# Kernel optimization log

Measured on AMD Instinct MI355X. Metric: run time of the kernel, lower is better.

The kernel has to match this reference:

```python
import jax, jax.numpy as jnp
import numpy as np

B, N, C, NH = 4, 2304, 256, 8
HD = C // NH            # head dim = 32
HS = WS = 48            # H = W = sqrt(N)
RADIUS = 3.0
MLP_HID = 4 * C
SCALE = HD ** (-0.5)
NEG = -1e9              # stands in for -inf (identical softmax up to fp eps)
EPS = 1e-6


def spatial_mask():
    # get_spatial_mask: cdist of (y, x) grid coords, -inf where dist > radius
    yy, xx = jnp.meshgrid(jnp.arange(HS), jnp.arange(WS), indexing='ij')
    coords = jnp.stack([yy, xx], -1).reshape(-1, 2).astype(jnp.float32)  # [N, 2]
    d2 = jnp.sum((coords[:, None, :] - coords[None, :, :]) ** 2, -1)     # [N, N]
    return jnp.where(d2 > RADIUS * RADIUS, NEG, 0.0)


def layernorm(x, g, b):
    mu = jnp.mean(x, -1, keepdims=True)
    var = jnp.mean((x - mu) ** 2, -1, keepdims=True)
    return (x - mu) * jax.lax.rsqrt(var + EPS) * g + b


def setup_inputs() -> dict:
    key = jax.random.key(0)
    ks = jax.random.split(key, 16)
    s = 0.02
    return {
        'x':    jax.random.normal(ks[0], (B, N, C), jnp.float32),
        'x_kv': jax.random.normal(ks[1], (B, N, C), jnp.float32),
        'Wq': jax.random.normal(ks[2], (C, C), jnp.float32) * s,
        'bq': jnp.zeros((C,), jnp.float32),
        'Wk': jax.random.normal(ks[3], (C, C), jnp.float32) * s,
        'bk': jnp.zeros((C,), jnp.float32),
        'Wv': jax.random.normal(ks[4], (C, C), jnp.float32) * s,
        'bv': jnp.zeros((C,), jnp.float32),
        'Wp': jax.random.normal(ks[5], (C, C), jnp.float32) * s,
        'bp': jnp.zeros((C,), jnp.float32),
        'g1': jnp.ones((C,), jnp.float32),
        'b1': jnp.zeros((C,), jnp.float32),
        'g2': jnp.ones((C,), jnp.float32),
        'b2': jnp.zeros((C,), jnp.float32),
        'W1': jax.random.normal(ks[6], (C, MLP_HID), jnp.float32) * s,
        'bm1': jnp.zeros((MLP_HID,), jnp.float32),
        'W2': jax.random.normal(ks[7], (MLP_HID, C), jnp.float32) * s,
        'bm2': jnp.zeros((C,), jnp.float32),
    }


def reference(x, x_kv, Wq, bq, Wk, bk, Wv, bv, Wp, bp,
              g1, b1, g2, b2, W1, bm1, W2, bm2):
    mask = spatial_mask()                                  # [N, N]
    h = layernorm(x, g1, b1)
    hkv = layernorm(x_kv, g1, b1)
    q = (h @ Wq + bq).reshape(B, N, NH, HD)
    k = (hkv @ Wk + bk).reshape(B, N, NH, HD)
    v = (hkv @ Wv + bv).reshape(B, N, NH, HD)
    scores = jnp.einsum('bqhd,bkhd->bhqk', q, k) * SCALE + mask
    attn = jax.nn.softmax(scores, axis=-1)
    out = jnp.einsum('bhqk,bkhd->bqhd', attn, v).reshape(B, N, C)
    x = x + out @ Wp + bp
    m = layernorm(x, g2, b2)
    x = x + jax.nn.gelu(m @ W1 + bm1, approximate=False) @ W2 + bm2
    return x
```

## Files before the change

kernel.cpp:

```cpp
#include <hip/hip_runtime.h>
#include <hip/hip_fp16.h>
#include <math.h>

#define BB 4
#define NN 2304
#define CC 256
#define HS 48
#define HID 1024
#define BNROWS (BB * NN)
#define ATTN_SCALE 0.17677669529663687f

typedef _Float16 f16;
typedef __attribute__((ext_vector_type(2))) _Float16 h2;
typedef __attribute__((ext_vector_type(8))) _Float16 h8;
typedef __attribute__((ext_vector_type(4))) float f4;

#define GLLS16(g, l)                                                        \
    __builtin_amdgcn_global_load_lds(                                       \
        (const __attribute__((address_space(1))) unsigned int*)(g),         \
        (__attribute__((address_space(3))) unsigned int*)(l), 16, 0, 0)
#define WAIT_VM0()   asm volatile("s_waitcnt vmcnt(0)" ::: "memory")
#define WAIT_VM6()   asm volatile("s_waitcnt vmcnt(6)" ::: "memory")
#define WAIT_LGKM0() asm volatile("s_waitcnt lgkmcnt(0)" ::: "memory")

static __device__ __forceinline__ float wave_sum64(float v) {
    v += __shfl_xor(v, 32, 64);
    v += __shfl_xor(v, 16, 64);
    v += __shfl_xor(v, 8, 64);
    v += __shfl_xor(v, 4, 64);
    v += __shfl_xor(v, 2, 64);
    v += __shfl_xor(v, 1, 64);
    return v;
}

static __device__ __forceinline__ int xcd_swizzle_lin() {
    const int gx = (int)gridDim.x;
    const int lin = (int)blockIdx.y * gx + (int)blockIdx.x;
    const int nwg = gx * (int)gridDim.y;
    return (nwg & 7) ? lin : ((lin & 7) * (nwg >> 3) + (lin >> 3));
}

__global__ __launch_bounds__(256) void prep_ln1_kernel(
    const float* __restrict__ x, const float* __restrict__ xkv,
    const float* __restrict__ Wq, const float* __restrict__ Wk,
    const float* __restrict__ Wv, const float* __restrict__ Wp,
    const float* __restrict__ W1, const float* __restrict__ W2,
    const float* __restrict__ bq, const float* __restrict__ bk,
    const float* __restrict__ bv,
    const float* __restrict__ g, const float* __restrict__ be,
    f16* __restrict__ WqkvT, f16* __restrict__ WpT,
    f16* __restrict__ W1T, f16* __restrict__ W2T, float* __restrict__ bqkv,
    f16* __restrict__ hq, f16* __restrict__ hkv)
{
    __shared__ float tt[32][33];
    int bx = blockIdx.x;
    const int tid = threadIdx.x;
    if (bx < 768) {
        const float* src; f16* dst; int K, N;
        if (bx < 64)        { src = Wq; dst = WqkvT;           K = 256;  N = 256; }
        else if (bx < 128)  { src = Wk; dst = WqkvT + 65536;   K = 256;  N = 256;  bx -= 64; }
        else if (bx < 192)  { src = Wv; dst = WqkvT + 131072;  K = 256;  N = 256;  bx -= 128; }
        else if (bx < 256)  { src = Wp; dst = WpT;             K = 256;  N = 256;  bx -= 192; }
        else if (bx < 512)  { src = W1; dst = W1T;             K = 256;  N = 1024; bx -= 256; }
        else                { src = W2; dst = W2T;             K = 1024; N = 256;  bx -= 512; }
        const int tN = N >> 5;
        const int kt = bx / tN, nt = bx - kt * tN;
        const int rr = tid >> 5, cc = tid & 31;
#pragma unroll
        for (int j = 0; j < 4; ++j)
            tt[rr + 8 * j][cc] = src[(size_t)(kt * 32 + rr + 8 * j) * N + nt * 32 + cc];
        __syncthreads();
#pragma unroll
        for (int j = 0; j < 4; ++j)
            dst[(size_t)(nt * 32 + rr + 8 * j) * K + kt * 32 + cc] = (f16)tt[cc][rr + 8 * j];
        return;
    }
    if (bx == 768) {
        if (tid < 256) {
            bqkv[tid]       = bq[tid];
            bqkv[tid + 256] = bk[tid];
            bqkv[tid + 512] = bv[tid];
        }
        return;
    }
    const int r = (bx - 769) * 4 + (tid >> 6);
    const int lane = tid & 63;
    const float* src; f16* dst;
    if (r < BNROWS) { src = x + (size_t)r * CC;              dst = hq + (size_t)r * CC; }
    else { src = xkv + (size_t)(r - BNROWS) * CC; dst = hkv + (size_t)(r - BNROWS) * CC; }
    const float4 v = ((const float4*)src)[lane];
    const float mu = wave_sum64(v.x + v.y + v.z + v.w) * (1.0f / CC);
    const float d0 = v.x - mu, d1 = v.y - mu, d2 = v.z - mu, d3 = v.w - mu;
    const float var = wave_sum64(d0 * d0 + d1 * d1 + d2 * d2 + d3 * d3) * (1.0f / CC);
    const float rs = rsqrtf(var + 1e-6f);
    const float4 g4 = ((const float4*)g)[lane];
    const float4 b4 = ((const float4*)be)[lane];
    h2 o01 = (h2){(f16)(d0 * rs * g4.x + b4.x), (f16)(d1 * rs * g4.y + b4.y)};
    h2 o23 = (h2){(f16)(d2 * rs * g4.z + b4.z), (f16)(d3 * rs * g4.w + b4.w)};
    ((h2*)dst)[lane * 2] = o01;
    ((h2*)dst)[lane * 2 + 1] = o23;
}

template <bool GELU, int RESID, bool OUTF32, bool QKV>
__global__ __launch_bounds__(256, 4) void gemm_wave(
    const f16* __restrict__ Aq, const f16* __restrict__ Akv,
    const f16* __restrict__ Bt, const float* __restrict__ bias,
    const void* __restrict__ resid, void* __restrict__ out1,
    void* __restrict__ outkv, int N, int K)
{
    __shared__ f16 lds[4 * 6144];
    const int tid = threadIdx.x;
    const int wid = tid >> 6, lane = tid & 63;
    const int ln15 = lane & 15, quad = lane >> 4;
    const int jr = lane >> 2, js = lane & 3;
    f16* slot = lds + wid * 6144;
    const int sl = xcd_swizzle_lin();
    const int gx = (int)gridDim.x;
    const int bx = sl % gx, by = sl / gx;
    const int n0 = bx * 64;
    const int m0 = (by * 4 + wid) * 32;
    const f16* Ap = QKV ? (n0 < 256 ? Aq : Akv) : Aq;

    size_t ga[2], gb[4];
#pragma unroll
    for (int i = 0; i < 2; ++i) {
        const int r = i * 16 + jr;
        const int q = (js - (r >> 1)) & 3;
        ga[i] = (size_t)(m0 + r) * K + q * 8;
    }
#pragma unroll
    for (int i = 0; i < 4; ++i) {
        const int r = i * 16 + jr;
        const int q = (js - (r >> 1)) & 3;
        gb[i] = (size_t)(n0 + r) * K + q * 8;
    }
    int aoff[2], boff[4];
#pragma unroll
    for (int mt = 0; mt < 2; ++mt) {
        const int r = mt * 16 + ln15;
        aoff[mt] = (r * 4 + ((quad + (r >> 1)) & 3)) * 16;
    }
#pragma unroll
    for (int nt = 0; nt < 4; ++nt) {
        const int r = nt * 16 + ln15;
        boff[nt] = (r * 4 + ((quad + (r >> 1)) & 3)) * 16;
    }

    f4 acc[2][4];
#pragma unroll
    for (int i = 0; i < 2; ++i)
#pragma unroll
        for (int j = 0; j < 4; ++j) acc[i][j] = (f4){0.f, 0.f, 0.f, 0.f};

    {
        f16* Al = slot;
        f16* Bl = slot + 1024;
#pragma unroll
        for (int i = 0; i < 2; ++i) GLLS16(Ap + ga[i], Al + i * 512);
#pragma unroll
        for (int i = 0; i < 4; ++i) GLLS16(Bt + gb[i], Bl + i * 512);
    }

    int cur = 0;
    for (int k0 = 0; k0 < K; k0 += 32) {
        const bool more = (k0 + 32 < K);
        f16* Ac = slot + cur * 3072;
        f16* Bc = Ac + 1024;
        if (more) {
            f16* An = slot + (cur ^ 1) * 3072;
            f16* Bn = An + 1024;
            WAIT_LGKM0();
#pragma unroll
            for (int i = 0; i < 2; ++i) GLLS16(Ap + ga[i] + k0 + 32, An + i * 512);
#pragma unroll
            for (int i = 0; i < 4; ++i) GLLS16(Bt + gb[i] + k0 + 32, Bn + i * 512);
            WAIT_VM6();
        } else {
            WAIT_VM0();
        }
        h8 aF[2], bF[4];
#pragma unroll
        for (int nt = 0; nt < 4; ++nt)
            bF[nt] = *(const h8*)((const char*)Bc + boff[nt]);
#pragma unroll
        for (int mt = 0; mt < 2; ++mt)
            aF[mt] = *(const h8*)((const char*)Ac + aoff[mt]);
#pragma unroll
        for (int mt = 0; mt < 2; ++mt)
#pragma unroll
            for (int nt = 0; nt < 4; ++nt)
                acc[mt][nt] = __builtin_amdgcn_mfma_f32_16x16x32_f16(
                    aF[mt], bF[nt], acc[mt][nt], 0, 0, 0);
        cur ^= 1;
    }

    f16* qdst = nullptr; int qstr = 0, qn0 = 0;
    if (QKV) {
        if (n0 < 256) { qdst = (f16*)out1;  qstr = 256; qn0 = n0; }
        else          { qdst = (f16*)outkv; qstr = 512; qn0 = n0 - 256; }
    }
#pragma unroll
    for (int nt = 0; nt < 4; ++nt) {
        const int gn = n0 + nt * 16 + ln15;
        const float bs = bias[gn];
#pragma unroll
        for (int mt = 0; mt < 2; ++mt) {
#pragma unroll
            for (int r = 0; r < 4; ++r) {
                const int gm = m0 + mt * 16 + quad * 4 + r;
                float v = acc[mt][nt][r] + bs;
                if (GELU) v = 0.5f * v * (1.0f + erff(v * 0.70710678118654752f));
                if (RESID == 1) v += ((const float*)resid)[(size_t)gm * N + gn];
                if (RESID == 2) v += (float)((const f16*)resid)[(size_t)gm * N + gn];
                if (QKV) {
                    qdst[(size_t)gm * qstr + qn0 + nt * 16 + ln15] = (f16)v;
                } else if (OUTF32) {
                    ((float*)out1)[(size_t)gm * N + gn] = v;
                } else {
                    ((f16*)out1)[(size_t)gm * N + gn] = (f16)v;
                }
            }
        }
    }
}

__global__ __launch_bounds__(256, 3) void gemm_op_ln2(
    const f16* __restrict__ Aa, const f16* __restrict__ Bt,
    const float* __restrict__ bias, const float* __restrict__ xres,
    const float* __restrict__ g, const float* __restrict__ be,
    f16* __restrict__ x1, f16* __restrict__ m2)
{
    __shared__ f16 lds[4 * 6144];
    __shared__ float sred[32][4][2];
    const int tid = threadIdx.x;
    const int wid = tid >> 6, lane = tid & 63;
    const int ln15 = lane & 15, quad = lane >> 4;
    const int jr = lane >> 2, js = lane & 3;
    f16* slot = lds + wid * 6144;
    const int m0 = blockIdx.x * 32;
    const int n0 = wid * 64;
    const int K = 256;

    size_t ga[2], gb[4];
#pragma unroll
    for (int i = 0; i < 2; ++i) {
        const int r = i * 16 + jr;
        const int q = (js - (r >> 1)) & 3;
        ga[i] = (size_t)(m0 + r) * K + q * 8;
    }
#pragma unroll
    for (int i = 0; i < 4; ++i) {
        const int r = i * 16 + jr;
        const int q = (js - (r >> 1)) & 3;
        gb[i] = (size_t)(n0 + r) * K + q * 8;
    }
    int aoff[2], boff[4];
#pragma unroll
    for (int mt = 0; mt < 2; ++mt) {
        const int r = mt * 16 + ln15;
        aoff[mt] = (r * 4 + ((quad + (r >> 1)) & 3)) * 16;
    }
#pragma unroll
    for (int nt = 0; nt < 4; ++nt) {
        const int r = nt * 16 + ln15;
        boff[nt] = (r * 4 + ((quad + (r >> 1)) & 3)) * 16;
    }

    f4 acc[2][4];
#pragma unroll
    for (int i = 0; i < 2; ++i)
#pragma unroll
        for (int j = 0; j < 4; ++j) acc[i][j] = (f4){0.f, 0.f, 0.f, 0.f};

    {
        f16* Al = slot;
        f16* Bl = slot + 1024;
#pragma unroll
        for (int i = 0; i < 2; ++i) GLLS16(Aa + ga[i], Al + i * 512);
#pragma unroll
        for (int i = 0; i < 4; ++i) GLLS16(Bt + gb[i], Bl + i * 512);
    }
    int cur = 0;
    for (int k0 = 0; k0 < K; k0 += 32) {
        const bool more = (k0 + 32 < K);
        f16* Ac = slot + cur * 3072;
        f16* Bc = Ac + 1024;
        if (more) {
            f16* An = slot + (cur ^ 1) * 3072;
            f16* Bn = An + 1024;
            WAIT_LGKM0();
#pragma unroll
            for (int i = 0; i < 2; ++i) GLLS16(Aa + ga[i] + k0 + 32, An + i * 512);
#pragma unroll
            for (int i = 0; i < 4; ++i) GLLS16(Bt + gb[i] + k0 + 32, Bn + i * 512);
            WAIT_VM6();
        } else {
            WAIT_VM0();
        }
        h8 aF[2], bF[4];
#pragma unroll
        for (int nt = 0; nt < 4; ++nt)
            bF[nt] = *(const h8*)((const char*)Bc + boff[nt]);
#pragma unroll
        for (int mt = 0; mt < 2; ++mt)
            aF[mt] = *(const h8*)((const char*)Ac + aoff[mt]);
#pragma unroll
        for (int mt = 0; mt < 2; ++mt)
#pragma unroll
            for (int nt = 0; nt < 4; ++nt)
                acc[mt][nt] = __builtin_amdgcn_mfma_f32_16x16x32_f16(
                    aF[mt], bF[nt], acc[mt][nt], 0, 0, 0);
        cur ^= 1;
    }

    float bsv[4], g2v[4], b2v[4];
#pragma unroll
    for (int nt = 0; nt < 4; ++nt) {
        const int gn = n0 + nt * 16 + ln15;
        bsv[nt] = bias[gn];
        g2v[nt] = g[gn];
        b2v[nt] = be[gn];
    }
    float s1[2][4], s2[2][4];
#pragma unroll
    for (int mt = 0; mt < 2; ++mt)
#pragma unroll
        for (int r = 0; r < 4; ++r) { s1[mt][r] = 0.f; s2[mt][r] = 0.f; }
#pragma unroll
    for (int mt = 0; mt < 2; ++mt) {
#pragma unroll
        for (int r = 0; r < 4; ++r) {
            const int gm = m0 + mt * 16 + quad * 4 + r;
#pragma unroll
            for (int nt = 0; nt < 4; ++nt) {
                const int gn = n0 + nt * 16 + ln15;
                float v = acc[mt][nt][r] + bsv[nt]
                        + xres[(size_t)gm * CC + gn];
                acc[mt][nt][r] = v;
                x1[(size_t)gm * CC + gn] = (f16)v;
                s1[mt][r] += v;
                s2[mt][r] += v * v;
            }
        }
    }
#pragma unroll
    for (int off = 1; off < 16; off <<= 1) {
#pragma unroll
        for (int mt = 0; mt < 2; ++mt)
#pragma unroll
            for (int r = 0; r < 4; ++r) {
                s1[mt][r] += __shfl_xor(s1[mt][r], off, 64);
                s2[mt][r] += __shfl_xor(s2[mt][r], off, 64);
            }
    }
    if (ln15 == 0) {
#pragma unroll
        for (int mt = 0; mt < 2; ++mt)
#pragma unroll
            for (int r = 0; r < 4; ++r) {
                const int rr = mt * 16 + quad * 4 + r;
                sred[rr][wid][0] = s1[mt][r];
                sred[rr][wid][1] = s2[mt][r];
            }
    }
    __syncthreads();
#pragma unroll
    for (int mt = 0; mt < 2; ++mt) {
#pragma unroll
        for (int r = 0; r < 4; ++r) {
            const int rr = mt * 16 + quad * 4 + r;
            const int gm = m0 + rr;
            float a = 0.f, b = 0.f;
#pragma unroll
            for (int w = 0; w < 4; ++w) {
                a += sred[rr][w][0];
                b += sred[rr][w][1];
            }
            const float mu = a * (1.0f / CC);
            const float var = fmaxf(b * (1.0f / CC) - mu * mu, 0.0f);
            const float rs = rsqrtf(var + 1e-6f);
#pragma unroll
            for (int nt = 0; nt < 4; ++nt) {
                const int gn = n0 + nt * 16 + ln15;
                const float v = acc[mt][nt][r];
                m2[(size_t)gm * CC + gn] =
                    (f16)((v - mu) * rs * g2v[nt] + b2v[nt]);
            }
        }
    }
}

__device__ __constant__ int ATT_DY[29] = {
    -3, -2, -2, -2, -2, -2, -1, -1, -1, -1, -1, 0, 0, 0, 0,
    0, 0, 0, 1, 1, 1, 1, 1, 2, 2, 2, 2, 2, 3};
__device__ __constant__ int ATT_DX[29] = {
    0, -2, -1, 0, 1, 2, -2, -1, 0, 1, 2, -3, -2, -1, 0,
    1, 2, 3, -2, -1, 0, 1, 2, -2, -1, 0, 1, 2, 0};

__global__ __launch_bounds__(128) void attn_tile_kernel(
    const f16* __restrict__ qf, const f16* __restrict__ kvf,
    f16* __restrict__ ao)
{
    __shared__ f16 ks[196][66];
    __shared__ f16 vs[196][66];
    const int tile = blockIdx.x, hp = blockIdx.y, b = blockIdx.z;
    const int ty0 = (tile / 6) * 8, tx0 = (tile - (tile / 6) * 6) * 8;
    const int tid = threadIdx.x;

    const int q = tid & 63, hh = tid >> 6;
    const int qy = q >> 3, qx = q & 7;
    const size_t qrow = (size_t)b * NN + (ty0 + qy) * HS + tx0 + qx;
    const f16* qp = qf + qrow * CC + hp * 64 + hh * 32;
    uint4 qa[4];
#pragma unroll
    for (int i = 0; i < 4; ++i) qa[i] = ((const uint4*)qp)[i];

#pragma unroll
    for (int bt = 0; bt < 5; ++bt) {
        uint4 v[5];
        int rr[5], sg[5];
#pragma unroll
        for (int j = 0; j < 5; ++j) {
            const int it = bt * 5 + j;
            const int idx = tid + it * 128;
            const int r = idx >> 4, seg = idx & 15;
            rr[j] = r; sg[j] = seg;
            const int ry = r / 14;
            const int gy = ty0 - 3 + ry, gx = tx0 - 3 + (r - ry * 14);
            uint4 val = {0u, 0u, 0u, 0u};
            const bool act = (it < 24) || (tid < 64);
            if (act && (unsigned)gy < HS && (unsigned)gx < HS) {
                const size_t rowb = ((size_t)b * NN + gy * HS + gx) * 512;
                const int ch = (seg < 8) ? (hp * 64 + seg * 8)
                                         : (256 + hp * 64 + (seg - 8) * 8);
                val = *(const uint4*)&kvf[rowb + ch];
            }
            v[j] = val;
        }
#pragma unroll
        for (int j = 0; j < 5; ++j) {
            const int it = bt * 5 + j;
            if (it == 24 && tid >= 64) continue;
            f16* dstp = (sg[j] < 8) ? &ks[rr[j]][(sg[j] & 7) * 8]
                                    : &vs[rr[j]][(sg[j] & 7) * 8];
            ((unsigned int*)dstp)[0] = v[j].x;
            ((unsigned int*)dstp)[1] = v[j].y;
            ((unsigned int*)dstp)[2] = v[j].z;
            ((unsigned int*)dstp)[3] = v[j].w;
        }
    }
    __syncthreads();

    const h2* q2 = (const h2*)qa;

    float s[29];
#pragma unroll
    for (int n = 0; n < 29; ++n) {
        const int dy = ATT_DY[n], dx = ATT_DX[n];
        const int r = (qy + 3 + dy) * 14 + qx + 3 + dx;
        const bool valid = (unsigned)(ty0 + qy + dy) < HS &&
                           (unsigned)(tx0 + qx + dx) < HS;
        float a = 0.0f;
        const h2* kp = (const h2*)&ks[r][hh * 32];
#pragma unroll
        for (int i = 0; i < 16; ++i)
            a = __builtin_amdgcn_fdot2(q2[i], kp[i], a, false);
        s[n] = valid ? a * ATTN_SCALE : -1e30f;
    }
    float m = s[0];
#pragma unroll
    for (int n = 1; n < 29; ++n) m = fmaxf(m, s[n]);
    float l = 0.0f;
#pragma unroll
    for (int n = 0; n < 29; ++n) { s[n] = __expf(s[n] - m); l += s[n]; }
    h2 a2[16];
#pragma unroll
    for (int i = 0; i < 16; ++i) a2[i] = (h2){(f16)0.f, (f16)0.f};
#pragma unroll
    for (int n = 0; n < 29; ++n) {
        const int dy = ATT_DY[n], dx = ATT_DX[n];
        const int r = (qy + 3 + dy) * 14 + qx + 3 + dx;
        const f16 pn = (f16)s[n];
        const h2 ph = (h2){pn, pn};
        const h2* vp = (const h2*)&vs[r][hh * 32];
#pragma unroll
        for (int i = 0; i < 16; ++i) a2[i] += ph * vp[i];
    }
    const float inv = 1.0f / l;
    uint4 ov[4];
    f16* oh = (f16*)ov;
#pragma unroll
    for (int i = 0; i < 16; ++i) {
        oh[2 * i]     = (f16)((float)a2[i][0] * inv);
        oh[2 * i + 1] = (f16)((float)a2[i][1] * inv);
    }
    uint4* dst = (uint4*)(ao + qrow * CC + hp * 64 + hh * 32);
#pragma unroll
    for (int i = 0; i < 4; ++i) dst[i] = ov[i];
}

extern "C" void kernel_launch(void* const* d_in, const int* in_sizes, int n_in,
                              void* d_out, int out_size, void* d_ws, size_t ws_size,
                              hipStream_t stream) {
    const float* x    = (const float*)d_in[0];
    const float* x_kv = (const float*)d_in[1];
    const float* Wq   = (const float*)d_in[2];
    const float* bq   = (const float*)d_in[3];
    const float* Wk   = (const float*)d_in[4];
    const float* bk   = (const float*)d_in[5];
    const float* Wv   = (const float*)d_in[6];
    const float* bv   = (const float*)d_in[7];
    const float* Wp   = (const float*)d_in[8];
    const float* bp   = (const float*)d_in[9];
    const float* g1   = (const float*)d_in[10];
    const float* b1   = (const float*)d_in[11];
    const float* g2   = (const float*)d_in[12];
    const float* b2   = (const float*)d_in[13];
    const float* W1   = (const float*)d_in[14];
    const float* bm1  = (const float*)d_in[15];
    const float* W2   = (const float*)d_in[16];
    const float* bm2  = (const float*)d_in[17];
    float* outp = (float*)d_out;

    f16* wsh = (f16*)d_ws;
    f16* WqkvT = wsh;
    f16* WpT   = wsh + 196608;
    f16* W1T   = wsh + 262144;
    f16* W2T   = wsh + 524288;
    float* bqkv = (float*)(wsh + 786432);
    f16* hq    = wsh + 787968;
    f16* hkv   = wsh + 3147264;
    f16* qf    = wsh + 5506560;
    f16* kvf   = wsh + 7865856;
    f16* ao    = hq;
    f16* x1    = hkv;
    f16* m2    = qf;
    f16* hidF  = kvf;
    const bool fused = ws_size >= (size_t)17303040 * sizeof(f16);

    prep_ln1_kernel<<<5377, 256, 0, stream>>>(
        x, x_kv, Wq, Wk, Wv, Wp, W1, W2, bq, bk, bv, g1, b1,
        WqkvT, WpT, W1T, W2T, bqkv, hq, hkv);
    gemm_wave<false, 0, false, true><<<dim3(12, 72), 256, 0, stream>>>(
        hq, hkv, WqkvT, bqkv, nullptr, qf, kvf, 768, 256);
    attn_tile_kernel<<<dim3(36, 4, BB), 128, 0, stream>>>(qf, kvf, ao);
    gemm_op_ln2<<<288, 256, 0, stream>>>(ao, WpT, bp, x, g2, b2, x1, m2);
    if (fused) {
        gemm_wave<true, 0, false, false><<<dim3(16, 72), 256, 0, stream>>>(
            m2, nullptr, W1T, bm1, nullptr, hidF, nullptr, 1024, 256);
        gemm_wave<false, 2, true, false><<<dim3(4, 72), 256, 0, stream>>>(
            hidF, nullptr, W2T, bm2, x1, outp, nullptr, 256, 1024);
    } else {
        for (int b = 0; b < BB; ++b) {
            const size_t off = (size_t)b * NN * CC;
            gemm_wave<true, 0, false, false><<<dim3(16, 18), 256, 0, stream>>>(
                m2 + off, nullptr, W1T, bm1, nullptr, hidF, nullptr, 1024, 256);
            gemm_wave<false, 2, true, false><<<dim3(4, 18), 256, 0, stream>>>(
                hidF, nullptr, W2T, bm2, x1 + off, outp + off, nullptr, 256, 1024);
        }
    }
    (void)in_sizes; (void)n_in; (void)out_size;
}
```

Baseline: 183.8 us.

## Fuse MLP up/down GEMMs keeping GELU hidden in LDS; shrink op-proj row tile

Replaces the two separate MLP GEMM launches with a single kernel. For each 32-row block it computes the W1 GEMM plus GELU in two 512-column halves, stores the hidden activations in swizzled LDS, and immediately feeds them into the W2 GEMM with the residual add. This removes the global write and re-read of the 4x-wide hidden tensor and one launch. The output-projection+LN2 kernel also moves from 32-row to 16-row tiles, doubling its block count and raising its occupancy hint. In exchange, the fused kernel uses more LDS, has only 288 blocks (low parallelism on a large GPU), and reloads W1/W2 for every row block.

```diff
diff --git a/kernel.cpp b/kernel.cpp
--- a/kernel.cpp
+++ b/kernel.cpp
@@ -20,6 +20,8 @@
         (const __attribute__((address_space(1))) unsigned int*)(g),         \
         (__attribute__((address_space(3))) unsigned int*)(l), 16, 0, 0)
 #define WAIT_VM0()   asm volatile("s_waitcnt vmcnt(0)" ::: "memory")
+#define WAIT_VM4()   asm volatile("s_waitcnt vmcnt(4)" ::: "memory")
+#define WAIT_VM5()   asm volatile("s_waitcnt vmcnt(5)" ::: "memory")
 #define WAIT_VM6()   asm volatile("s_waitcnt vmcnt(6)" ::: "memory")
 #define WAIT_LGKM0() asm volatile("s_waitcnt lgkmcnt(0)" ::: "memory")
 
@@ -224,35 +226,181 @@
     }
 }
 
-__global__ __launch_bounds__(256, 3) void gemm_op_ln2(
+__global__ __launch_bounds__(256, 4) void gemm_op_ln2(
     const f16* __restrict__ Aa, const f16* __restrict__ Bt,
     const float* __restrict__ bias, const float* __restrict__ xres,
     const float* __restrict__ g, const float* __restrict__ be,
     f16* __restrict__ x1, f16* __restrict__ m2)
 {
+    __shared__ f16 lds[4 * 5120];
+    __shared__ float sred[16][4][2];
+    const int tid = threadIdx.x;
+    const int wid = tid >> 6, lane = tid & 63;
+    const int ln15 = lane & 15, quad = lane >> 4;
+    const int jr = lane >> 2, js = lane & 3;
+    f16* slot = lds + wid * 5120;
+    const int m0 = blockIdx.x * 16;
+    const int n0 = wid * 64;
+    const int K = 256;
+
+    size_t ga, gb[4];
+    {
+        const int q = (js - (jr >> 1)) & 3;
+        ga = (size_t)(m0 + jr) * K + q * 8;
+    }
+#pragma unroll
+    for (int i = 0; i < 4; ++i) {
+        const int r = i * 16 + jr;
+        const int q = (js - (r >> 1)) & 3;
+        gb[i] = (size_t)(n0 + r) * K + q * 8;
+    }
+    const int aoff = (ln15 * 4 + ((quad + (ln15 >> 1)) & 3)) * 16;
+    int boff[4];
+#pragma unroll
+    for (int nt = 0; nt < 4; ++nt) {
+        const int r = nt * 16 + ln15;
+        boff[nt] = (r * 4 + ((quad + (r >> 1)) & 3)) * 16;
+    }
+
+    f4 acc[4];
+#pragma unroll
+    for (int j = 0; j < 4; ++j) acc[j] = (f4){0.f, 0.f, 0.f, 0.f};
+
+    {
+        f16* Al = slot;
+        f16* Bl = slot + 512;
+        GLLS16(Aa + ga, Al);
+#pragma unroll
+        for (int i = 0; i < 4; ++i) GLLS16(Bt + gb[i], Bl + i * 512);
+    }
+    int cur = 0;
+    for (int k0 = 0; k0 < K; k0 += 32) {
+        const bool more = (k0 + 32 < K);
+        f16* Ac = slot + cur * 2560;
+        f16* Bc = Ac + 512;
+        if (more) {
+            f16* An = slot + (cur ^ 1) * 2560;
+            f16* Bn = An + 512;
+            WAIT_LGKM0();
+            GLLS16(Aa + ga + k0 + 32, An);
+#pragma unroll
+            for (int i = 0; i < 4; ++i) GLLS16(Bt + gb[i] + k0 + 32, Bn + i * 512);
+            WAIT_VM5();
+        } else {
+            WAIT_VM0();
+        }
+        h8 aF, bF[4];
+#pragma unroll
+        for (int nt = 0; nt < 4; ++nt)
+            bF[nt] = *(const h8*)((const char*)Bc + boff[nt]);
+        aF = *(const h8*)((const char*)Ac + aoff);
+#pragma unroll
+        for (int nt = 0; nt < 4; ++nt)
+            acc[nt] = __builtin_amdgcn_mfma_f32_16x16x32_f16(
+                aF, bF[nt], acc[nt], 0, 0, 0);
+        cur ^= 1;
+    }
+
+    float bsv[4], g2v[4], b2v[4];
+#pragma unroll
+    for (int nt = 0; nt < 4; ++nt) {
+        const int gn = n0 + nt * 16 + ln15;
+        bsv[nt] = bias[gn];
+        g2v[nt] = g[gn];
+        b2v[nt] = be[gn];
+    }
+    float s1[4], s2[4];
+#pragma unroll
+    for (int r = 0; r < 4; ++r) { s1[r] = 0.f; s2[r] = 0.f; }
+#pragma unroll
+    for (int r = 0; r < 4; ++r) {
+        const int gm = m0 + quad * 4 + r;
+#pragma unroll
+        for (int nt = 0; nt < 4; ++nt) {
+            const int gn = n0 + nt * 16 + ln15;
+            float v = acc[nt][r] + bsv[nt] + xres[(size_t)gm * CC + gn];
+            acc[nt][r] = v;
+            x1[(size_t)gm * CC + gn] = (f16)v;
+            s1[r] += v;
+            s2[r] += v * v;
+        }
+    }
+#pragma unroll
+    for (int off = 1; off < 16; off <<= 1) {
+#pragma unroll
+        for (int r = 0; r < 4; ++r) {
+            s1[r] += __shfl_xor(s1[r], off, 64);
+            s2[r] += __shfl_xor(s2[r], off, 64);
+        }
+    }
+    if (ln15 == 0) {
+#pragma unroll
+        for (int r = 0; r < 4; ++r) {
+            const int rr = quad * 4 + r;
+            sred[rr][wid][0] = s1[r];
+            sred[rr][wid][1] = s2[r];
+        }
+    }
+    __syncthreads();
+#pragma unroll
+    for (int r = 0; r < 4; ++r) {
+        const int rr = quad * 4 + r;
+        const int gm = m0 + rr;
+        float a = 0.f, b = 0.f;
+#pragma unroll
+        for (int w = 0; w < 4; ++w) {
+            a += sred[rr][w][0];
+            b += sred[rr][w][1];
+        }
+        const float mu = a * (1.0f / CC);
+        const float var = fmaxf(b * (1.0f / CC) - mu * mu, 0.0f);
+        const float rs = rsqrtf(var + 1e-6f);
+#pragma unroll
+        for (int nt = 0; nt < 4; ++nt) {
+            const int gn = n0 + nt * 16 + ln15;
+            const float v = acc[nt][r];
+            m2[(size_t)gm * CC + gn] = (f16)((v - mu) * rs * g2v[nt] + b2v[nt]);
+        }
+    }
+}
+
+__global__ __launch_bounds__(256, 2) void mlp_fused(
+    const f16* __restrict__ m2g, const f16* __restrict__ W1T,
+    const f16* __restrict__ W2T, const float* __restrict__ bm1,
+    const float* __restrict__ bm2, const f16* __restrict__ x1,
+    float* __restrict__ outp)
+{
     __shared__ f16 lds[4 * 6144];
-    __shared__ float sred[32][4][2];
+    __shared__ f16 hbuf[32 * 512];
     const int tid = threadIdx.x;
     const int wid = tid >> 6, lane = tid & 63;
     const int ln15 = lane & 15, quad = lane >> 4;
     const int jr = lane >> 2, js = lane & 3;
     f16* slot = lds + wid * 6144;
     const int m0 = blockIdx.x * 32;
-    const int n0 = wid * 64;
-    const int K = 256;
-
-    size_t ga[2], gb[4];
+
+    size_t ga[2];
 #pragma unroll
     for (int i = 0; i < 2; ++i) {
         const int r = i * 16 + jr;
         const int q = (js - (r >> 1)) & 3;
-        ga[i] = (size_t)(m0 + r) * K + q * 8;
-    }
+        ga[i] = (size_t)(m0 + r) * 256 + q * 8;
+    }
+    size_t gb1[2][4];
+#pragma unroll
+    for (int nt2 = 0; nt2 < 2; ++nt2)
+#pragma unroll
+        for (int i = 0; i < 4; ++i) {
+            const int r = i * 16 + jr;
+            const int q = (js - (r >> 1)) & 3;
+            gb1[nt2][i] = (size_t)(wid * 128 + nt2 * 64 + r) * 256 + q * 8;
+        }
+    size_t gb2[4];
 #pragma unroll
     for (int i = 0; i < 4; ++i) {
         const int r = i * 16 + jr;
         const int q = (js - (r >> 1)) & 3;
-        gb[i] = (size_t)(n0 + r) * K + q * 8;
+        gb2[i] = (size_t)(wid * 64 + r) * 1024 + q * 8;
     }
     int aoff[2], boff[4];
 #pragma unroll
@@ -266,125 +414,136 @@
         boff[nt] = (r * 4 + ((quad + (r >> 1)) & 3)) * 16;
     }
 
-    f4 acc[2][4];
+    f4 acc2[2][4];
 #pragma unroll
     for (int i = 0; i < 2; ++i)
 #pragma unroll
-        for (int j = 0; j < 4; ++j) acc[i][j] = (f4){0.f, 0.f, 0.f, 0.f};
-
-    {
-        f16* Al = slot;
-        f16* Bl = slot + 1024;
-#pragma unroll
-        for (int i = 0; i < 2; ++i) GLLS16(Aa + ga[i], Al + i * 512);
-#pragma unroll
-        for (int i = 0; i < 4; ++i) GLLS16(Bt + gb[i], Bl + i * 512);
-    }
-    int cur = 0;
-    for (int k0 = 0; k0 < K; k0 += 32) {
-        const bool more = (k0 + 32 < K);
-        f16* Ac = slot + cur * 3072;
-        f16* Bc = Ac + 1024;
-        if (more) {
-            f16* An = slot + (cur ^ 1) * 3072;
-            f16* Bn = An + 1024;
-            WAIT_LGKM0();
-#pragma unroll
-            for (int i = 0; i < 2; ++i) GLLS16(Aa + ga[i] + k0 + 32, An + i * 512);
-#pragma unroll
-            for (int i = 0; i < 4; ++i) GLLS16(Bt + gb[i] + k0 + 32, Bn + i * 512);
-            WAIT_VM6();
-        } else {
-            WAIT_VM0();
-        }
-        h8 aF[2], bF[4];
-#pragma unroll
-        for (int nt = 0; nt < 4; ++nt)
-            bF[nt] = *(const h8*)((const char*)Bc + boff[nt]);
-#pragma unroll
-        for (int mt = 0; mt < 2; ++mt)
-            aF[mt] = *(const h8*)((const char*)Ac + aoff[mt]);
-#pragma unroll
-        for (int mt = 0; mt < 2; ++mt)
+        for (int j = 0; j < 4; ++j) acc2[i][j] = (f4){0.f, 0.f, 0.f, 0.f};
+
+#pragma unroll 1
+    for (int half = 0; half < 2; ++half) {
+        const size_t bofs1 = (size_t)half * 512 * 256;
+        {
+            f16* Al = slot;
+            f16* Bl = slot + 1024;
+#pragma unroll
+            for (int i = 0; i < 2; ++i) GLLS16(m2g + ga[i], Al + i * 512);
+#pragma unroll
+            for (int i = 0; i < 4; ++i) GLLS16(W1T + gb1[0][i] + bofs1, Bl + i * 512);
+        }
+        int cur = 0;
+        f4 accp[2][4];
+#pragma unroll 1
+        for (int it = 0; it < 16; ++it) {
+            const int ntile = it >> 3;
+            f16* Ac = slot + cur * 3072;
+            f16* Bc = Ac + 1024;
+            if (it < 15) {
+                const int itn = it + 1;
+                const int ntn = itn >> 3, k0n = (itn & 7) * 32;
+                f16* An = slot + (cur ^ 1) * 3072;
+                f16* Bn = An + 1024;
+                WAIT_LGKM0();
+#pragma unroll
+                for (int i = 0; i < 2; ++i)
+                    GLLS16(m2g + ga[i] + k0n, An + i * 512);
+#pragma unroll
+                for (int i = 0; i < 4; ++i)
+                    GLLS16(W1T + gb1[ntn][i] + bofs1 + k0n, Bn + i * 512);
+                WAIT_VM6();
+            } else {
+                WAIT_VM0();
+            }
+            if ((it & 7) == 0) {
+#pragma unroll
+                for (int i = 0; i < 2; ++i)
+#pragma unroll
+                    for (int j = 0; j < 4; ++j) accp[i][j] = (f4){0.f, 0.f, 0.f, 0.f};
+            }
+            h8 aF[2], bF[4];
 #pragma unroll
             for (int nt = 0; nt < 4; ++nt)
-                acc[mt][nt] = __builtin_amdgcn_mfma_f32_16x16x32_f16(
-                    aF[mt], bF[nt], acc[mt][nt], 0, 0, 0);
-        cur ^= 1;
-    }
-
-    float bsv[4], g2v[4], b2v[4];
+                bF[nt] = *(const h8*)((const char*)Bc + boff[nt]);
+#pragma unroll
+            for (int mt = 0; mt < 2; ++mt)
+                aF[mt] = *(const h8*)((const char*)Ac + aoff[mt]);
+#pragma unroll
+            for (int mt = 0; mt < 2; ++mt)
+#pragma unroll
+                for (int nt = 0; nt < 4; ++nt)
+                    accp[mt][nt] = __builtin_amdgcn_mfma_f32_16x16x32_f16(
+                        aF[mt], bF[nt], accp[mt][nt], 0, 0, 0);
+            if ((it & 7) == 7) {
+#pragma unroll
+                for (int mt = 0; mt < 2; ++mt)
+#pragma unroll
+                    for (int nt = 0; nt < 4; ++nt)
+#pragma unroll
+                        for (int r = 0; r < 4; ++r) {
+                            const int row = mt * 16 + quad * 4 + r;
+                            const int col = wid * 128 + ntile * 64 + nt * 16 + ln15;
+                            float v = accp[mt][nt][r] + bm1[half * 512 + col];
+                            v = 0.5f * v * (1.0f + erff(v * 0.70710678118654752f));
+                            const int sw = (col >> 3) ^ (row & 7);
+                            hbuf[row * 512 + sw * 8 + (col & 7)] = (f16)v;
+                        }
+            }
+            cur ^= 1;
+        }
+        __syncthreads();
+        {
+            f16* Bl = slot;
+#pragma unroll
+            for (int i = 0; i < 4; ++i)
+                GLLS16(W2T + gb2[i] + half * 512, Bl + i * 512);
+        }
+        cur = 0;
+#pragma unroll 1
+        for (int it = 0; it < 16; ++it) {
+            f16* Bc = slot + cur * 2048;
+            if (it < 15) {
+                f16* Bn = slot + (cur ^ 1) * 2048;
+                WAIT_LGKM0();
+#pragma unroll
+                for (int i = 0; i < 4; ++i)
+                    GLLS16(W2T + gb2[i] + half * 512 + (it + 1) * 32, Bn + i * 512);
+                WAIT_VM4();
+            } else {
+                WAIT_VM0();
+            }
+            h8 bF[4];
+#pragma unroll
+            for (int nt = 0; nt < 4; ++nt)
+                bF[nt] = *(const h8*)((const char*)Bc + boff[nt]);
+            h8 aF[2];
+#pragma unroll
+            for (int mt = 0; mt < 2; ++mt) {
+                const int row = mt * 16 + ln15;
+                const int sw = (it * 4 + quad) ^ (row & 7);
+                aF[mt] = *(const h8*)&hbuf[row * 512 + sw * 8];
+            }
+#pragma unroll
+            for (int mt = 0; mt < 2; ++mt)
+#pragma unroll
+                for (int nt = 0; nt < 4; ++nt)
+                    acc2[mt][nt] = __builtin_amdgcn_mfma_f32_16x16x32_f16(
+                        aF[mt], bF[nt], acc2[mt][nt], 0, 0, 0);
+            cur ^= 1;
+        }
+        if (half == 0) __syncthreads();
+    }
 #pragma unroll
     for (int nt = 0; nt < 4; ++nt) {
-        const int gn = n0 + nt * 16 + ln15;
-        bsv[nt] = bias[gn];
-        g2v[nt] = g[gn];
-        b2v[nt] = be[gn];
-    }
-    float s1[2][4], s2[2][4];
-#pragma unroll
-    for (int mt = 0; mt < 2; ++mt)
-#pragma unroll
-        for (int r = 0; r < 4; ++r) { s1[mt][r] = 0.f; s2[mt][r] = 0.f; }
-#pragma unroll
-    for (int mt = 0; mt < 2; ++mt) {
-#pragma unroll
-        for (int r = 0; r < 4; ++r) {
-            const int gm = m0 + mt * 16 + quad * 4 + r;
-#pragma unroll
-            for (int nt = 0; nt < 4; ++nt) {
-                const int gn = n0 + nt * 16 + ln15;
-                float v = acc[mt][nt][r] + bsv[nt]
-                        + xres[(size_t)gm * CC + gn];
-                acc[mt][nt][r] = v;
-                x1[(size_t)gm * CC + gn] = (f16)v;
-                s1[mt][r] += v;
-                s2[mt][r] += v * v;
-            }
-        }
-    }
-#pragma unroll
-    for (int off = 1; off < 16; off <<= 1) {
-#pragma unroll
-        for (int mt = 0; mt < 2; ++mt)
+        const int gn = wid * 64 + nt * 16 + ln15;
+        const float bs = bm2[gn];
+#pragma unroll
+        for (int mt = 0; mt < 2; ++mt) {
 #pragma unroll
             for (int r = 0; r < 4; ++r) {
-                s1[mt][r] += __shfl_xor(s1[mt][r], off, 64);
-                s2[mt][r] += __shfl_xor(s2[mt][r], off, 64);
-            }
-    }
-    if (ln15 == 0) {
-#pragma unroll
-        for (int mt = 0; mt < 2; ++mt)
-#pragma unroll
-            for (int r = 0; r < 4; ++r) {
-                const int rr = mt * 16 + quad * 4 + r;
-                sred[rr][wid][0] = s1[mt][r];
-                sred[rr][wid][1] = s2[mt][r];
-            }
-    }
-    __syncthreads();
-#pragma unroll
-    for (int mt = 0; mt < 2; ++mt) {
-#pragma unroll
-        for (int r = 0; r < 4; ++r) {
-            const int rr = mt * 16 + quad * 4 + r;
-            const int gm = m0 + rr;
-            float a = 0.f, b = 0.f;
-#pragma unroll
-            for (int w = 0; w < 4; ++w) {
-                a += sred[rr][w][0];
-                b += sred[rr][w][1];
-            }
-            const float mu = a * (1.0f / CC);
-            const float var = fmaxf(b * (1.0f / CC) - mu * mu, 0.0f);
-            const float rs = rsqrtf(var + 1e-6f);
-#pragma unroll
-            for (int nt = 0; nt < 4; ++nt) {
-                const int gn = n0 + nt * 16 + ln15;
-                const float v = acc[mt][nt][r];
-                m2[(size_t)gm * CC + gn] =
-                    (f16)((v - mu) * rs * g2v[nt] + b2v[nt]);
+                const int gm = m0 + mt * 16 + quad * 4 + r;
+                const float v = acc2[mt][nt][r] + bs
+                              + (float)x1[(size_t)gm * CC + gn];
+                outp[(size_t)gm * CC + gn] = v;
             }
         }
     }
@@ -535,8 +694,6 @@
     f16* ao    = hq;
     f16* x1    = hkv;
     f16* m2    = qf;
-    f16* hidF  = kvf;
-    const bool fused = ws_size >= (size_t)17303040 * sizeof(f16);
 
     prep_ln1_kernel<<<5377, 256, 0, stream>>>(
         x, x_kv, Wq, Wk, Wv, Wp, W1, W2, bq, bk, bv, g1, b1,
@@ -544,20 +701,7 @@
     gemm_wave<false, 0, false, true><<<dim3(12, 72), 256, 0, stream>>>(
         hq, hkv, WqkvT, bqkv, nullptr, qf, kvf, 768, 256);
     attn_tile_kernel<<<dim3(36, 4, BB), 128, 0, stream>>>(qf, kvf, ao);
-    gemm_op_ln2<<<288, 256, 0, stream>>>(ao, WpT, bp, x, g2, b2, x1, m2);
-    if (fused) {
-        gemm_wave<true, 0, false, false><<<dim3(16, 72), 256, 0, stream>>>(
-            m2, nullptr, W1T, bm1, nullptr, hidF, nullptr, 1024, 256);
-        gemm_wave<false, 2, true, false><<<dim3(4, 72), 256, 0, stream>>>(
-            hidF, nullptr, W2T, bm2, x1, outp, nullptr, 256, 1024);
-    } else {
-        for (int b = 0; b < BB; ++b) {
-            const size_t off = (size_t)b * NN * CC;
-            gemm_wave<true, 0, false, false><<<dim3(16, 18), 256, 0, stream>>>(
-                m2 + off, nullptr, W1T, bm1, nullptr, hidF, nullptr, 1024, 256);
-            gemm_wave<false, 2, true, false><<<dim3(4, 18), 256, 0, stream>>>(
-                hidF, nullptr, W2T, bm2, x1 + off, outp + off, nullptr, 256, 1024);
-        }
-    }
-    (void)in_sizes; (void)n_in; (void)out_size;
+    gemm_op_ln2<<<576, 256, 0, stream>>>(ao, WpT, bp, x, g2, b2, x1, m2);
+    mlp_fused<<<288, 256, 0, stream>>>(m2, W1T, W2T, bm1, bm2, x1, outp);
+    (void)in_sizes; (void)n_in; (void)out_size; (void)ws_size;
 }
```

Measured after the change: 185.7 us. Within noise of the previous version (+1.0%).

## Replace per-wave GEMM tiles with block-cooperative shared LDS tiles

Applied to the files above, without the earlier changes.

Replaces the per-wave private 32x64 GEMM tiles with a templated block-level GEMM in which all four waves cooperatively stage a shared BMxBN tile (128x128 or 128x64) into LDS, synchronised with __syncthreads. Tile data is then reused across waves, cutting redundant global and LDS-fill traffic for the QKV, MLP1 and MLP2 GEMMs. The out-projection+LN2 GEMM is folded into the same template. The change swaps the fine-grained per-wave vmcnt/lgkmcnt waits for block barriers, which may add stall time, and larger tiles mean fewer workgroups, which may reduce occupancy.

```diff
diff --git a/kernel.cpp b/kernel.cpp
--- a/kernel.cpp
+++ b/kernel.cpp
@@ -19,9 +19,6 @@
     __builtin_amdgcn_global_load_lds(                                       \
         (const __attribute__((address_space(1))) unsigned int*)(g),         \
         (__attribute__((address_space(3))) unsigned int*)(l), 16, 0, 0)
-#define WAIT_VM0()   asm volatile("s_waitcnt vmcnt(0)" ::: "memory")
-#define WAIT_VM6()   asm volatile("s_waitcnt vmcnt(6)" ::: "memory")
-#define WAIT_LGKM0() asm volatile("s_waitcnt lgkmcnt(0)" ::: "memory")
 
 static __device__ __forceinline__ float wave_sum64(float v) {
     v += __shfl_xor(v, 32, 64);
@@ -101,290 +98,193 @@
     ((h2*)dst)[lane * 2 + 1] = o23;
 }
 
-template <bool GELU, int RESID, bool OUTF32, bool QKV>
-__global__ __launch_bounds__(256, 4) void gemm_wave(
+template <int BM, int BN, int WGM, int WGN, int EPI>
+__global__ __launch_bounds__(256, 3) void gemm_block(
     const f16* __restrict__ Aq, const f16* __restrict__ Akv,
     const f16* __restrict__ Bt, const float* __restrict__ bias,
-    const void* __restrict__ resid, void* __restrict__ out1,
-    void* __restrict__ outkv, int N, int K)
+    const void* __restrict__ resid, const float* __restrict__ lng,
+    const float* __restrict__ lnb, void* __restrict__ out1,
+    void* __restrict__ out2, int N, int K)
 {
-    __shared__ f16 lds[4 * 6144];
-    const int tid = threadIdx.x;
-    const int wid = tid >> 6, lane = tid & 63;
-    const int ln15 = lane & 15, quad = lane >> 4;
-    const int jr = lane >> 2, js = lane & 3;
-    f16* slot = lds + wid * 6144;
-    const int sl = xcd_swizzle_lin();
-    const int gx = (int)gridDim.x;
-    const int bx = sl % gx, by = sl / gx;
-    const int n0 = bx * 64;
-    const int m0 = (by * 4 + wid) * 32;
-    const f16* Ap = QKV ? (n0 < 256 ? Aq : Akv) : Aq;
-
-    size_t ga[2], gb[4];
-#pragma unroll
-    for (int i = 0; i < 2; ++i) {
-        const int r = i * 16 + jr;
-        const int q = (js - (r >> 1)) & 3;
-        ga[i] = (size_t)(m0 + r) * K + q * 8;
-    }
-#pragma unroll
-    for (int i = 0; i < 4; ++i) {
-        const int r = i * 16 + jr;
-        const int q = (js - (r >> 1)) & 3;
-        gb[i] = (size_t)(n0 + r) * K + q * 8;
-    }
-    int aoff[2], boff[4];
-#pragma unroll
-    for (int mt = 0; mt < 2; ++mt) {
-        const int r = mt * 16 + ln15;
-        aoff[mt] = (r * 4 + ((quad + (r >> 1)) & 3)) * 16;
-    }
-#pragma unroll
-    for (int nt = 0; nt < 4; ++nt) {
-        const int r = nt * 16 + ln15;
-        boff[nt] = (r * 4 + ((quad + (r >> 1)) & 3)) * 16;
-    }
-
-    f4 acc[2][4];
-#pragma unroll
-    for (int i = 0; i < 2; ++i)
-#pragma unroll
-        for (int j = 0; j < 4; ++j) acc[i][j] = (f4){0.f, 0.f, 0.f, 0.f};
-
-    {
-        f16* Al = slot;
-        f16* Bl = slot + 1024;
-#pragma unroll
-        for (int i = 0; i < 2; ++i) GLLS16(Ap + ga[i], Al + i * 512);
-#pragma unroll
-        for (int i = 0; i < 4; ++i) GLLS16(Bt + gb[i], Bl + i * 512);
-    }
-
-    int cur = 0;
-    for (int k0 = 0; k0 < K; k0 += 32) {
-        const bool more = (k0 + 32 < K);
-        f16* Ac = slot + cur * 3072;
-        f16* Bc = Ac + 1024;
-        if (more) {
-            f16* An = slot + (cur ^ 1) * 3072;
-            f16* Bn = An + 1024;
-            WAIT_LGKM0();
-#pragma unroll
-            for (int i = 0; i < 2; ++i) GLLS16(Ap + ga[i] + k0 + 32, An + i * 512);
-#pragma unroll
-            for (int i = 0; i < 4; ++i) GLLS16(Bt + gb[i] + k0 + 32, Bn + i * 512);
-            WAIT_VM6();
-        } else {
-            WAIT_VM0();
-        }
-        h8 aF[2], bF[4];
-#pragma unroll
-        for (int nt = 0; nt < 4; ++nt)
-            bF[nt] = *(const h8*)((const char*)Bc + boff[nt]);
-#pragma unroll
-        for (int mt = 0; mt < 2; ++mt)
-            aF[mt] = *(const h8*)((const char*)Ac + aoff[mt]);
-#pragma unroll
-        for (int mt = 0; mt < 2; ++mt)
-#pragma unroll
-            for (int nt = 0; nt < 4; ++nt)
-                acc[mt][nt] = __builtin_amdgcn_mfma_f32_16x16x32_f16(
-                    aF[mt], bF[nt], acc[mt][nt], 0, 0, 0);
-        cur ^= 1;
-    }
-
-    f16* qdst = nullptr; int qstr = 0, qn0 = 0;
-    if (QKV) {
-        if (n0 < 256) { qdst = (f16*)out1;  qstr = 256; qn0 = n0; }
-        else          { qdst = (f16*)outkv; qstr = 512; qn0 = n0 - 256; }
-    }
-#pragma unroll
-    for (int nt = 0; nt < 4; ++nt) {
-        const int gn = n0 + nt * 16 + ln15;
-        const float bs = bias[gn];
-#pragma unroll
-        for (int mt = 0; mt < 2; ++mt) {
-#pragma unroll
-            for (int r = 0; r < 4; ++r) {
-                const int gm = m0 + mt * 16 + quad * 4 + r;
-                float v = acc[mt][nt][r] + bs;
-                if (GELU) v = 0.5f * v * (1.0f + erff(v * 0.70710678118654752f));
-                if (RESID == 1) v += ((const float*)resid)[(size_t)gm * N + gn];
-                if (RESID == 2) v += (float)((const f16*)resid)[(size_t)gm * N + gn];
-                if (QKV) {
-                    qdst[(size_t)gm * qstr + qn0 + nt * 16 + ln15] = (f16)v;
-                } else if (OUTF32) {
-                    ((float*)out1)[(size_t)gm * N + gn] = v;
-                } else {
-                    ((f16*)out1)[(size_t)gm * N + gn] = (f16)v;
-                }
-            }
-        }
-    }
-}
-
-__global__ __launch_bounds__(256, 3) void gemm_op_ln2(
-    const f16* __restrict__ Aa, const f16* __restrict__ Bt,
-    const float* __restrict__ bias, const float* __restrict__ xres,
-    const float* __restrict__ g, const float* __restrict__ be,
-    f16* __restrict__ x1, f16* __restrict__ m2)
-{
-    __shared__ f16 lds[4 * 6144];
+    constexpr int A_G = BM / 16, B_G = BN / 16, T = A_G + B_G;
+    constexpr int BUFE = (BM + BN) * 32;
+    constexpr int WM = BM / WGM, WN = BN / WGN;
+    constexpr int MT = WM / 16;
+    __shared__ f16 lds[2 * BUFE];
     __shared__ float sred[32][4][2];
     const int tid = threadIdx.x;
     const int wid = tid >> 6, lane = tid & 63;
     const int ln15 = lane & 15, quad = lane >> 4;
     const int jr = lane >> 2, js = lane & 3;
-    f16* slot = lds + wid * 6144;
-    const int m0 = blockIdx.x * 32;
-    const int n0 = wid * 64;
-    const int K = 256;
-
-    size_t ga[2], gb[4];
-#pragma unroll
-    for (int i = 0; i < 2; ++i) {
-        const int r = i * 16 + jr;
-        const int q = (js - (r >> 1)) & 3;
-        ga[i] = (size_t)(m0 + r) * K + q * 8;
-    }
-#pragma unroll
-    for (int i = 0; i < 4; ++i) {
-        const int r = i * 16 + jr;
-        const int q = (js - (r >> 1)) & 3;
-        gb[i] = (size_t)(n0 + r) * K + q * 8;
-    }
-    int aoff[2], boff[4];
-#pragma unroll
-    for (int mt = 0; mt < 2; ++mt) {
-        const int r = mt * 16 + ln15;
-        aoff[mt] = (r * 4 + ((quad + (r >> 1)) & 3)) * 16;
+    const int wr = wid / WGN, wc = wid % WGN;
+
+    const int sl = xcd_swizzle_lin();
+    const int gx = (int)gridDim.x;
+    const int m0 = (sl % gx) * BM;
+    const int n0 = (sl / gx) * BN;
+    const f16* A = (EPI == 0) ? (n0 < 256 ? Aq : Akv) : Aq;
+
+    const size_t gabase = (size_t)jr * K + (size_t)(((js - (jr >> 1)) & 3) * 8);
+
+    int aoff[MT], boff[4];
+#pragma unroll
+    for (int mt = 0; mt < MT; ++mt) {
+        const int rr = wr * WM + mt * 16 + ln15;
+        aoff[mt] = (rr * 4 + ((quad + (rr >> 1)) & 3)) * 16;
     }
 #pragma unroll
     for (int nt = 0; nt < 4; ++nt) {
-        const int r = nt * 16 + ln15;
-        boff[nt] = (r * 4 + ((quad + (r >> 1)) & 3)) * 16;
-    }
-
-    f4 acc[2][4];
-#pragma unroll
-    for (int i = 0; i < 2; ++i)
+        const int rr = wc * WN + nt * 16 + ln15;
+        boff[nt] = BM * 64 + (rr * 4 + ((quad + (rr >> 1)) & 3)) * 16;
+    }
+
+    f4 acc[MT][4];
+#pragma unroll
+    for (int i = 0; i < MT; ++i)
 #pragma unroll
         for (int j = 0; j < 4; ++j) acc[i][j] = (f4){0.f, 0.f, 0.f, 0.f};
 
-    {
-        f16* Al = slot;
-        f16* Bl = slot + 1024;
-#pragma unroll
-        for (int i = 0; i < 2; ++i) GLLS16(Aa + ga[i], Al + i * 512);
-#pragma unroll
-        for (int i = 0; i < 4; ++i) GLLS16(Bt + gb[i], Bl + i * 512);
-    }
+#define GB_STAGE(dst, kk)                                                     \
+    _Pragma("unroll")                                                         \
+    for (int i = 0; i < (T + 3) / 4; ++i) {                                   \
+        const int g = wid + i * 4;                                            \
+        if (g < T) {                                                          \
+            const bool isB = (g >= A_G);                                      \
+            const size_t rowoff =                                             \
+                (size_t)(isB ? (n0 + (g - A_G) * 16) : (m0 + g * 16)) * K;    \
+            const f16* sp = (isB ? Bt : A) + rowoff + gabase + (kk);          \
+            GLLS16(sp, (dst) + g * 512);                                      \
+        }                                                                     \
+    }
+
+    GB_STAGE(lds, 0);
+    __syncthreads();
     int cur = 0;
     for (int k0 = 0; k0 < K; k0 += 32) {
-        const bool more = (k0 + 32 < K);
-        f16* Ac = slot + cur * 3072;
-        f16* Bc = Ac + 1024;
-        if (more) {
-            f16* An = slot + (cur ^ 1) * 3072;
-            f16* Bn = An + 1024;
-            WAIT_LGKM0();
-#pragma unroll
-            for (int i = 0; i < 2; ++i) GLLS16(Aa + ga[i] + k0 + 32, An + i * 512);
-#pragma unroll
-            for (int i = 0; i < 4; ++i) GLLS16(Bt + gb[i] + k0 + 32, Bn + i * 512);
-            WAIT_VM6();
-        } else {
-            WAIT_VM0();
-        }
-        h8 aF[2], bF[4];
+        f16* bufc = lds + cur * BUFE;
+        if (k0 + 32 < K) { GB_STAGE(lds + (cur ^ 1) * BUFE, k0 + 32); }
+        h8 aF[MT], bF[4];
 #pragma unroll
         for (int nt = 0; nt < 4; ++nt)
-            bF[nt] = *(const h8*)((const char*)Bc + boff[nt]);
-#pragma unroll
-        for (int mt = 0; mt < 2; ++mt)
-            aF[mt] = *(const h8*)((const char*)Ac + aoff[mt]);
-#pragma unroll
-        for (int mt = 0; mt < 2; ++mt)
+            bF[nt] = *(const h8*)((const char*)bufc + boff[nt]);
+#pragma unroll
+        for (int mt = 0; mt < MT; ++mt)
+            aF[mt] = *(const h8*)((const char*)bufc + aoff[mt]);
+#pragma unroll
+        for (int mt = 0; mt < MT; ++mt)
 #pragma unroll
             for (int nt = 0; nt < 4; ++nt)
                 acc[mt][nt] = __builtin_amdgcn_mfma_f32_16x16x32_f16(
                     aF[mt], bF[nt], acc[mt][nt], 0, 0, 0);
+        __syncthreads();
         cur ^= 1;
     }
-
-    float bsv[4], g2v[4], b2v[4];
-#pragma unroll
-    for (int nt = 0; nt < 4; ++nt) {
-        const int gn = n0 + nt * 16 + ln15;
-        bsv[nt] = bias[gn];
-        g2v[nt] = g[gn];
-        b2v[nt] = be[gn];
-    }
-    float s1[2][4], s2[2][4];
-#pragma unroll
-    for (int mt = 0; mt < 2; ++mt)
-#pragma unroll
-        for (int r = 0; r < 4; ++r) { s1[mt][r] = 0.f; s2[mt][r] = 0.f; }
-#pragma unroll
-    for (int mt = 0; mt < 2; ++mt) {
-#pragma unroll
-        for (int r = 0; r < 4; ++r) {
-            const int gm = m0 + mt * 16 + quad * 4 + r;
-#pragma unroll
-            for (int nt = 0; nt < 4; ++nt) {
-                const int gn = n0 + nt * 16 + ln15;
-                float v = acc[mt][nt][r] + bsv[nt]
-                        + xres[(size_t)gm * CC + gn];
-                acc[mt][nt][r] = v;
-                x1[(size_t)gm * CC + gn] = (f16)v;
-                s1[mt][r] += v;
-                s2[mt][r] += v * v;
+#undef GB_STAGE
+
+    if constexpr (EPI == 3) {
+        const float* xres = (const float*)resid;
+        f16* x1 = (f16*)out1;
+        f16* m2 = (f16*)out2;
+        float bsv[4], gv[4], bv[4];
+#pragma unroll
+        for (int nt = 0; nt < 4; ++nt) {
+            const int gn = n0 + wc * WN + nt * 16 + ln15;
+            bsv[nt] = bias[gn]; gv[nt] = lng[gn]; bv[nt] = lnb[gn];
+        }
+        float s1[MT][4], s2[MT][4];
+#pragma unroll
+        for (int mt = 0; mt < MT; ++mt)
+#pragma unroll
+            for (int r = 0; r < 4; ++r) { s1[mt][r] = 0.f; s2[mt][r] = 0.f; }
+#pragma unroll
+        for (int mt = 0; mt < MT; ++mt) {
+#pragma unroll
+            for (int r = 0; r < 4; ++r) {
+                const int gm = m0 + mt * 16 + quad * 4 + r;
+#pragma unroll
+                for (int nt = 0; nt < 4; ++nt) {
+                    const int gn = n0 + wc * WN + nt * 16 + ln15;
+                    float v = acc[mt][nt][r] + bsv[nt]
+                            + xres[(size_t)gm * CC + gn];
+                    acc[mt][nt][r] = v;
+                    x1[(size_t)gm * CC + gn] = (f16)v;
+                    s1[mt][r] += v;
+                    s2[mt][r] += v * v;
+                }
             }
         }
-    }
-#pragma unroll
-    for (int off = 1; off < 16; off <<= 1) {
-#pragma unroll
-        for (int mt = 0; mt < 2; ++mt)
-#pragma unroll
-            for (int r = 0; r < 4; ++r) {
-                s1[mt][r] += __shfl_xor(s1[mt][r], off, 64);
-                s2[mt][r] += __shfl_xor(s2[mt][r], off, 64);
-            }
-    }
-    if (ln15 == 0) {
-#pragma unroll
-        for (int mt = 0; mt < 2; ++mt)
+#pragma unroll
+        for (int off = 1; off < 16; off <<= 1) {
+#pragma unroll
+            for (int mt = 0; mt < MT; ++mt)
+#pragma unroll
+                for (int r = 0; r < 4; ++r) {
+                    s1[mt][r] += __shfl_xor(s1[mt][r], off, 64);
+                    s2[mt][r] += __shfl_xor(s2[mt][r], off, 64);
+                }
+        }
+        if (ln15 == 0) {
+#pragma unroll
+            for (int mt = 0; mt < MT; ++mt)
+#pragma unroll
+                for (int r = 0; r < 4; ++r) {
+                    const int rr = mt * 16 + quad * 4 + r;
+                    sred[rr][wid][0] = s1[mt][r];
+                    sred[rr][wid][1] = s2[mt][r];
+                }
+        }
+        __syncthreads();
+#pragma unroll
+        for (int mt = 0; mt < MT; ++mt) {
 #pragma unroll
             for (int r = 0; r < 4; ++r) {
                 const int rr = mt * 16 + quad * 4 + r;
-                sred[rr][wid][0] = s1[mt][r];
-                sred[rr][wid][1] = s2[mt][r];
+                const int gm = m0 + rr;
+                float a = 0.f, b = 0.f;
+#pragma unroll
+                for (int w = 0; w < 4; ++w) {
+                    a += sred[rr][w][0];
+                    b += sred[rr][w][1];
+                }
+                const float mu = a * (1.0f / CC);
+                const float var = fmaxf(b * (1.0f / CC) - mu * mu, 0.0f);
+                const float rs = rsqrtf(var + 1e-6f);
+#pragma unroll
+                for (int nt = 0; nt < 4; ++nt) {
+                    const int gn = n0 + wc * WN + nt * 16 + ln15;
+                    const float v = acc[mt][nt][r];
+                    m2[(size_t)gm * CC + gn] =
+                        (f16)((v - mu) * rs * gv[nt] + bv[nt]);
+                }
             }
-    }
-    __syncthreads();
-#pragma unroll
-    for (int mt = 0; mt < 2; ++mt) {
-#pragma unroll
-        for (int r = 0; r < 4; ++r) {
-            const int rr = mt * 16 + quad * 4 + r;
-            const int gm = m0 + rr;
-            float a = 0.f, b = 0.f;
-#pragma unroll
-            for (int w = 0; w < 4; ++w) {
-                a += sred[rr][w][0];
-                b += sred[rr][w][1];
-            }
-            const float mu = a * (1.0f / CC);
-            const float var = fmaxf(b * (1.0f / CC) - mu * mu, 0.0f);
-            const float rs = rsqrtf(var + 1e-6f);
-#pragma unroll
-            for (int nt = 0; nt < 4; ++nt) {
-                const int gn = n0 + nt * 16 + ln15;
-                const float v = acc[mt][nt][r];
-                m2[(size_t)gm * CC + gn] =
-                    (f16)((v - mu) * rs * g2v[nt] + b2v[nt]);
+        }
+    } else {
+        f16* qdst = nullptr; int qstr = 0, qn0 = 0;
+        if constexpr (EPI == 0) {
+            if (n0 < 256) { qdst = (f16*)out1; qstr = 256; qn0 = n0; }
+            else          { qdst = (f16*)out2; qstr = 512; qn0 = n0 - 256; }
+        }
+#pragma unroll
+        for (int nt = 0; nt < 4; ++nt) {
+            const int cl = wc * WN + nt * 16 + ln15;
+            const int gn = n0 + cl;
+            const float bs = bias[gn];
+#pragma unroll
+            for (int mt = 0; mt < MT; ++mt) {
+#pragma unroll
+                for (int r = 0; r < 4; ++r) {
+                    const int gm = m0 + wr * WM + mt * 16 + quad * 4 + r;
+                    float v = acc[mt][nt][r] + bs;
+                    if constexpr (EPI == 0) {
+                        qdst[(size_t)gm * qstr + qn0 + cl] = (f16)v;
+                    } else if constexpr (EPI == 1) {
+                        v = 0.5f * v * (1.0f + erff(v * 0.70710678118654752f));
+                        ((f16*)out1)[(size_t)gm * N + gn] = (f16)v;
+                    } else {
+                        v += (float)((const f16*)resid)[(size_t)gm * N + gn];
+                        ((float*)out1)[(size_t)gm * N + gn] = v;
+                    }
+                }
             }
         }
     }
@@ -541,22 +441,27 @@
     prep_ln1_kernel<<<5377, 256, 0, stream>>>(
         x, x_kv, Wq, Wk, Wv, Wp, W1, W2, bq, bk, bv, g1, b1,
         WqkvT, WpT, W1T, W2T, bqkv, hq, hkv);
-    gemm_wave<false, 0, false, true><<<dim3(12, 72), 256, 0, stream>>>(
-        hq, hkv, WqkvT, bqkv, nullptr, qf, kvf, 768, 256);
+    gemm_block<128, 128, 2, 2, 0><<<dim3(72, 6), 256, 0, stream>>>(
+        hq, hkv, WqkvT, bqkv, nullptr, nullptr, nullptr, qf, kvf, 768, 256);
     attn_tile_kernel<<<dim3(36, 4, BB), 128, 0, stream>>>(qf, kvf, ao);
-    gemm_op_ln2<<<288, 256, 0, stream>>>(ao, WpT, bp, x, g2, b2, x1, m2);
+    gemm_block<32, 256, 1, 4, 3><<<dim3(288, 1), 256, 0, stream>>>(
+        ao, nullptr, WpT, bp, x, g2, b2, x1, m2, 256, 256);
     if (fused) {
-        gemm_wave<true, 0, false, false><<<dim3(16, 72), 256, 0, stream>>>(
-            m2, nullptr, W1T, bm1, nullptr, hidF, nullptr, 1024, 256);
-        gemm_wave<false, 2, true, false><<<dim3(4, 72), 256, 0, stream>>>(
-            hidF, nullptr, W2T, bm2, x1, outp, nullptr, 256, 1024);
+        gemm_block<128, 128, 2, 2, 1><<<dim3(72, 8), 256, 0, stream>>>(
+            m2, nullptr, W1T, bm1, nullptr, nullptr, nullptr, hidF, nullptr,
+            HID, 256);
+        gemm_block<128, 64, 4, 1, 2><<<dim3(72, 4), 256, 0, stream>>>(
+            hidF, nullptr, W2T, bm2, x1, nullptr, nullptr, outp, nullptr,
+            CC, 1024);
     } else {
         for (int b = 0; b < BB; ++b) {
             const size_t off = (size_t)b * NN * CC;
-            gemm_wave<true, 0, false, false><<<dim3(16, 18), 256, 0, stream>>>(
-                m2 + off, nullptr, W1T, bm1, nullptr, hidF, nullptr, 1024, 256);
-            gemm_wave<false, 2, true, false><<<dim3(4, 18), 256, 0, stream>>>(
-                hidF, nullptr, W2T, bm2, x1 + off, outp + off, nullptr, 256, 1024);
+            gemm_block<128, 128, 2, 2, 1><<<dim3(18, 8), 256, 0, stream>>>(
+                m2 + off, nullptr, W1T, bm1, nullptr, nullptr, nullptr, hidF,
+                nullptr, HID, 256);
+            gemm_block<128, 64, 4, 1, 2><<<dim3(18, 4), 256, 0, stream>>>(
+                hidF, nullptr, W2T, bm2, x1 + off, nullptr, nullptr,
+                outp + off, nullptr, CC, 1024);
         }
     }
     (void)in_sizes; (void)n_in; (void)out_size;
```

Result: no change. 184.2 us (+0.2%).
